# Kernel tuning notes

Measured on AMD Instinct MI355X. Metric: run time of the kernel, lower is better.

## Reference

```python
import jax, jax.numpy as jnp
import numpy as np

NUM_HEADS = 16
EPS = 1e-5
BLOCK = 16  # score_mod: q_idx // 16 == kv_idx % 16


def _ln(x, eps=EPS):
    # LayerNorm, elementwise_affine=False
    m = jnp.mean(x, axis=-1, keepdims=True)
    v = jnp.mean((x - m) ** 2, axis=-1, keepdims=True)
    return (x - m) * jax.lax.rsqrt(v + eps)


def setup_inputs() -> dict:
    key = jax.random.key(0)
    ks = jax.random.split(key, 5)
    N, D = 2048, 2048
    w = 0.02
    return {
        "x": jax.random.normal(ks[0], (N, D), jnp.float32),
        "Wq": jax.random.normal(ks[1], (D, D), jnp.float32) * w,
        "Wk": jax.random.normal(ks[2], (D, D), jnp.float32) * w,
        "Wv": jax.random.normal(ks[3], (D, D), jnp.float32) * w,
        "Wo": jax.random.normal(ks[4], (D, D), jnp.float32) * w,
    }


def reference(x, Wq, Wk, Wv, Wo):
    N, D = x.shape
    H = NUM_HEADS
    DH = D // H
    x_in = x
    xn = _ln(x)
    # per-head q/k layernorm, cast to attention dtype (bfloat16)
    q = _ln((xn @ Wq).reshape(N, H, DH)).astype(jnp.bfloat16)
    k = _ln((xn @ Wk).reshape(N, H, DH)).astype(jnp.bfloat16)
    v = (xn @ Wv).reshape(N, H, DH)  # stays fp32 (original applies no cast to vs)
    scale = 1.0 / np.sqrt(DH)
    # dense scores then sparsity mask, as flex_attention with score_mod does
    scores = jnp.einsum("nhd,mhd->hnm", q, k, preferred_element_type=jnp.float32) * scale
    qi = jnp.arange(N)
    mask = (qi[:, None] // BLOCK) == (qi[None, :] % BLOCK)  # [N, N]
    s = jnp.where(mask[None, :, :], scores, -jnp.inf)
    # safe softmax: rows with no allowed keys (q_idx >= 256) produce zeros
    mx = jnp.max(s, axis=-1, keepdims=True)
    e = jnp.exp(s - jnp.where(jnp.isfinite(mx), mx, 0.0))
    denom = jnp.sum(e, axis=-1, keepdims=True)
    attn = e / jnp.maximum(denom, 1e-30)
    o = jnp.einsum("hnm,mhd->nhd", attn, v)  # [N, H, DH]
    out = o.reshape(N, D) @ Wo
    return out + x_in
```

## Files before the change

### kernel.cpp

```cpp
#include <hip/hip_runtime.h>

typedef unsigned short u16;
typedef __attribute__((ext_vector_type(8))) short short8;
typedef __attribute__((ext_vector_type(4))) float f32x4;

#define D 2048
#define EPS 1e-5f

__device__ __forceinline__ u16 f2bf(float f) {
  unsigned u = __float_as_uint(f);
  u += 0x7fffu + ((u >> 16) & 1u);
  return (u16)(u >> 16);
}

__device__ __forceinline__ void async16(const void* g, void* l) {
  __builtin_amdgcn_global_load_lds(
      (const __attribute__((address_space(1))) void*)g,
      (__attribute__((address_space(3))) void*)l, 16, 0, 0);
}

__global__ __launch_bounds__(256) void prep(const float* __restrict__ x,
                                            const float* __restrict__ Wq,
                                            const float* __restrict__ Wk,
                                            const float* __restrict__ Wv,
                                            const float* __restrict__ Wo,
                                            u16* __restrict__ xn,
                                            float* __restrict__ out,
                                            u16* __restrict__ WqT, u16* __restrict__ WkT,
                                            u16* __restrict__ WvT, u16* __restrict__ WoT) {
  int bid = blockIdx.x;
  int t = threadIdx.x;
  if (bid < 2048) {
    const float* xr = x + (size_t)bid * D;
    float4 v[2];
    float s = 0.f, sq = 0.f;
#pragma unroll
    for (int i = 0; i < 2; i++) {
      v[i] = *(const float4*)(xr + i * 1024 + t * 4);
      s += v[i].x + v[i].y + v[i].z + v[i].w;
      sq += v[i].x * v[i].x + v[i].y * v[i].y + v[i].z * v[i].z + v[i].w * v[i].w;
    }
#pragma unroll
    for (int m = 32; m >= 1; m >>= 1) { s += __shfl_xor(s, m); sq += __shfl_xor(sq, m); }
    __shared__ float ps[4], pq[4];
    int w = t >> 6, lane = t & 63;
    if (lane == 0) { ps[w] = s; pq[w] = sq; }
    __syncthreads();
    s = ps[0] + ps[1] + ps[2] + ps[3];
    sq = pq[0] + pq[1] + pq[2] + pq[3];
    float mean = s * (1.f / D);
    float var = sq * (1.f / D) - mean * mean;
    float rs = rsqrtf(var + EPS);
    float* outr = out + (size_t)bid * D;
    u16* xnr = xn + (size_t)bid * D;
#pragma unroll
    for (int i = 0; i < 2; i++) {
      *(float4*)(outr + i * 1024 + t * 4) = v[i];
      ushort4 o;
      o.x = f2bf((v[i].x - mean) * rs);
      o.y = f2bf((v[i].y - mean) * rs);
      o.z = f2bf((v[i].z - mean) * rs);
      o.w = f2bf((v[i].w - mean) * rs);
      *(ushort4*)(xnr + i * 1024 + t * 4) = o;
    }
  } else {
    int tb = bid - 2048;
    int wsel = tb >> 10;
    int tt = tb & 1023;
    const float* src; u16* dst;
    switch (wsel) {
      case 0: src = Wq; dst = WqT; break;
      case 1: src = Wk; dst = WkT; break;
      case 2: src = Wv; dst = WvT; break;
      default: src = Wo; dst = WoT; break;
    }
    int i0 = (tt >> 5) * 64, j0 = (tt & 31) * 64;
    __shared__ u16 tile[64 * 66];
#pragma unroll
    for (int r = 0; r < 4; r++) {
      int idx = r * 256 + t;
      int row = idx >> 4, c4 = idx & 15;
      float4 v = *(const float4*)(src + (size_t)(i0 + row) * D + j0 + c4 * 4);
      tile[row * 66 + c4 * 4 + 0] = f2bf(v.x);
      tile[row * 66 + c4 * 4 + 1] = f2bf(v.y);
      tile[row * 66 + c4 * 4 + 2] = f2bf(v.z);
      tile[row * 66 + c4 * 4 + 3] = f2bf(v.w);
    }
    __syncthreads();
#pragma unroll
    for (int r = 0; r < 4; r++) {
      int idx = r * 256 + t;
      int row = idx >> 4, c4 = idx & 15;
      ushort4 o;
      o.x = tile[(c4 * 4 + 0) * 66 + row];
      o.y = tile[(c4 * 4 + 1) * 66 + row];
      o.z = tile[(c4 * 4 + 2) * 66 + row];
      o.w = tile[(c4 * 4 + 3) * 66 + row];
      *(ushort4*)(dst + (size_t)(j0 + row) * D + i0 + c4 * 4) = o;
    }
  }
}

__device__ __forceinline__ void gemm_tile(const u16* __restrict__ A,
                                          const u16* __restrict__ Bt,
                                          bool permB, int m0, int n0,
                                          int kbeg, int kend,
                                          u16* As, u16* Bs, f32x4 acc[4][4]) {
  int tid = threadIdx.x, wid = tid >> 6, lane = tid & 63;
  int q4 = lane >> 4, m16 = lane & 15;
  int wm = wid >> 1, wn = wid & 1;
  for (int kb = kbeg; kb < kend; kb += 64) {
#pragma unroll
    for (int p = 0; p < 4; p++) {
      int idx = p * 256 + tid;
      int r = idx >> 3, sl = idx & 7;
      int gc = sl ^ (r & 7);
      async16(A + (size_t)(m0 + r) * D + kb + gc * 8, As + (size_t)(p * 256 + wid * 64) * 8);
      int rb = n0 + r;
      int gr = permB ? ((rb & 127) * 16 + (rb >> 7)) : rb;
      async16(Bt + (size_t)gr * D + kb + gc * 8, Bs + (size_t)(p * 256 + wid * 64) * 8);
    }
    __syncthreads();
#pragma unroll
    for (int ks = 0; ks < 2; ks++) {
      short8 af[4], bf[4];
      int c = ks * 4 + q4;
#pragma unroll
      for (int i = 0; i < 4; i++) {
        int ra = wm * 64 + i * 16 + m16;
        af[i] = *(const short8*)(As + ra * 64 + (c ^ (ra & 7)) * 8);
        int rb = wn * 64 + i * 16 + m16;
        bf[i] = *(const short8*)(Bs + rb * 64 + (c ^ (rb & 7)) * 8);
      }
#pragma unroll
      for (int i = 0; i < 4; i++)
#pragma unroll
        for (int j = 0; j < 4; j++)
          acc[i][j] = __builtin_amdgcn_mfma_f32_16x16x32_bf16(af[i], bf[j], acc[i][j], 0, 0, 0);
    }
    __syncthreads();
  }
}

__global__ __launch_bounds__(256, 3) void gemm_mega(const u16* __restrict__ xn,
                                                    const u16* __restrict__ WkT,
                                                    const u16* __restrict__ WvT,
                                                    u16* __restrict__ K3,
                                                    u16* __restrict__ V3) {
  __shared__ u16 smem[2 * 128 * 64];
  u16* As = smem;
  u16* Bs = smem + 8192;
  int bid0 = blockIdx.x;
  int bid = (bid0 & 7) * 64 + (bid0 >> 3);
  int sel = bid >> 8;
  int z = bid & 255;
  int m0 = (z >> 4) * 128, n0 = (z & 15) * 128;
  const u16* A = sel ? WvT : xn;
  const u16* Bt = sel ? xn : WkT;
  f32x4 acc[4][4];
#pragma unroll
  for (int i = 0; i < 4; i++)
#pragma unroll
    for (int j = 0; j < 4; j++)
#pragma unroll
      for (int r = 0; r < 4; r++) acc[i][j][r] = 0.f;
  gemm_tile(A, Bt, sel == 1, m0, n0, 0, D, As, Bs, acc);

  int tid = threadIdx.x, wid = tid >> 6, lane = tid & 63;
  int q4 = lane >> 4, m16 = lane & 15;
  int wm = wid >> 1, wn = wid & 1;
  if (sel == 1) {
    int h = m0 >> 7, b = n0 >> 7;
#pragma unroll
    for (int i = 0; i < 4; i++)
#pragma unroll
      for (int j = 0; j < 4; j++)
#pragma unroll
        for (int r = 0; r < 4; r++) {
          int dhl = wm * 64 + i * 16 + q4 * 4 + r;
          int key = wn * 64 + j * 16 + m16;
          V3[((size_t)(h * 16 + b) * 128 + dhl) * 128 + key] = f2bf(acc[i][j][r]);
        }
  } else {
    float* redS = (float*)smem;
    float* redQ = redS + 256;
    __syncthreads();
#pragma unroll
    for (int i = 0; i < 4; i++) {
      float ps[4], pq[4];
#pragma unroll
      for (int r = 0; r < 4; r++) {
        float s = 0.f, q = 0.f;
#pragma unroll
        for (int j = 0; j < 4; j++) { float a = acc[i][j][r]; s += a; q += a * a; }
#pragma unroll
        for (int msk = 1; msk < 16; msk <<= 1) {
          s += __shfl_xor(s, msk);
          q += __shfl_xor(q, msk);
        }
        ps[r] = s; pq[r] = q;
      }
      if (m16 == 0) {
#pragma unroll
        for (int r = 0; r < 4; r++) {
          int row = wm * 64 + i * 16 + q4 * 4 + r;
          redS[row * 2 + wn] = ps[r];
          redQ[row * 2 + wn] = pq[r];
        }
      }
    }
    __syncthreads();
    int h = n0 >> 7;
#pragma unroll
    for (int i = 0; i < 4; i++)
#pragma unroll
      for (int r = 0; r < 4; r++) {
        int row = wm * 64 + i * 16 + q4 * 4 + r;
        float S = redS[row * 2] + redS[row * 2 + 1];
        float Qs = redQ[row * 2] + redQ[row * 2 + 1];
        float mean = S * (1.f / 128.f);
        float var = Qs * (1.f / 128.f) - mean * mean;
        float rstd = rsqrtf(var + EPS);
        int tok = m0 + row;
#pragma unroll
        for (int j = 0; j < 4; j++) {
          int dhl = wn * 64 + j * 16 + m16;
          u16 val = f2bf((acc[i][j][r] - mean) * rstd);
          K3[(((size_t)(h * 16 + (tok & 15))) * 128 + (tok >> 4)) * 128 + dhl] = val;
        }
      }
  }
}

__global__ __launch_bounds__(256) void attn(const u16* __restrict__ xn,
                                            const u16* __restrict__ WqT,
                                            const u16* __restrict__ K3,
                                            const u16* __restrict__ V3,
                                            u16* __restrict__ Ob) {
  int bh = blockIdx.x;
  int h = bh & 15, b = bh >> 4;
  int tid = threadIdx.x, w = tid >> 6, lane = tid & 63;
  int q4 = lane >> 4, m16 = lane & 15;
  __shared__ u16 Qs[16][136];
  __shared__ u16 P[16][136];
  __shared__ float redA[16][4];
  __shared__ float redB[16][4];
  __shared__ float redmx[4][16];
  __shared__ float redsm[4][16];
  __shared__ float invd[16];
  const float scale = 0.08838834764831845f;
  const u16* Ktile = K3 + (size_t)(h * 16 + b) * 128 * 128;
  const u16* Vtile = V3 + (size_t)(h * 16 + b) * 128 * 128;

  f32x4 qa[2];
#pragma unroll
  for (int nt = 0; nt < 2; nt++)
#pragma unroll
    for (int r = 0; r < 4; r++) qa[nt][r] = 0.f;
  const u16* xr = xn + (size_t)(b * 16 + m16) * D + q4 * 8;
  const u16* wr = WqT + (size_t)(h * 128 + w * 32 + m16) * D + q4 * 8;
#pragma unroll 4
  for (int kk = 0; kk < D; kk += 32) {
    short8 a = *(const short8*)(xr + kk);
    short8 b0 = *(const short8*)(wr + kk);
    short8 b1 = *(const short8*)(wr + 16 * D + kk);
    qa[0] = __builtin_amdgcn_mfma_f32_16x16x32_bf16(a, b0, qa[0], 0, 0, 0);
    qa[1] = __builtin_amdgcn_mfma_f32_16x16x32_bf16(a, b1, qa[1], 0, 0, 0);
  }
#pragma unroll
  for (int r = 0; r < 4; r++) {
    float s = qa[0][r] + qa[1][r];
    float q2 = qa[0][r] * qa[0][r] + qa[1][r] * qa[1][r];
#pragma unroll
    for (int msk = 1; msk < 16; msk <<= 1) { s += __shfl_xor(s, msk); q2 += __shfl_xor(q2, msk); }
    if (m16 == 0) { redA[q4 * 4 + r][w] = s; redB[q4 * 4 + r][w] = q2; }
  }
  __syncthreads();
#pragma unroll
  for (int r = 0; r < 4; r++) {
    int row = q4 * 4 + r;
    float S = redA[row][0] + redA[row][1] + redA[row][2] + redA[row][3];
    float Q2 = redB[row][0] + redB[row][1] + redB[row][2] + redB[row][3];
    float mean = S * (1.f / 128.f);
    float var = Q2 * (1.f / 128.f) - mean * mean;
    float rstd = rsqrtf(var + EPS);
#pragma unroll
    for (int nt = 0; nt < 2; nt++)
      Qs[row][w * 32 + nt * 16 + m16] = f2bf((qa[nt][r] - mean) * rstd);
  }
  __syncthreads();

  short8 af[4];
#pragma unroll
  for (int dc = 0; dc < 4; dc++)
    af[dc] = *(const short8*)(&Qs[m16][dc * 32 + q4 * 8]);
  f32x4 s[2];
#pragma unroll
  for (int kt = 0; kt < 2; kt++)
#pragma unroll
    for (int r = 0; r < 4; r++) s[kt][r] = 0.f;
#pragma unroll
  for (int kt = 0; kt < 2; kt++) {
    int key = w * 32 + kt * 16 + m16;
#pragma unroll
    for (int dc = 0; dc < 4; dc++) {
      short8 bf = *(const short8*)(Ktile + (size_t)key * 128 + dc * 32 + q4 * 8);
      s[kt] = __builtin_amdgcn_mfma_f32_16x16x32_bf16(af[dc], bf, s[kt], 0, 0, 0);
    }
  }
  float mx[4];
#pragma unroll
  for (int r = 0; r < 4; r++) {
    mx[r] = fmaxf(s[0][r], s[1][r]);
#pragma unroll
    for (int msk = 1; msk < 16; msk <<= 1) mx[r] = fmaxf(mx[r], __shfl_xor(mx[r], msk));
    if (m16 == 0) redmx[w][q4 * 4 + r] = mx[r];
  }
  __syncthreads();
#pragma unroll
  for (int r = 0; r < 4; r++) {
    int row = q4 * 4 + r;
    float M = fmaxf(fmaxf(redmx[0][row], redmx[1][row]), fmaxf(redmx[2][row], redmx[3][row]));
    float acc = 0.f;
#pragma unroll
    for (int kt = 0; kt < 2; kt++) {
      float e = __expf((s[kt][r] - M) * scale);
      s[kt][r] = e;
      acc += e;
    }
#pragma unroll
    for (int msk = 1; msk < 16; msk <<= 1) acc += __shfl_xor(acc, msk);
    if (m16 == 0) redsm[w][row] = acc;
  }
#pragma unroll
  for (int kt = 0; kt < 2; kt++)
#pragma unroll
    for (int r = 0; r < 4; r++)
      P[q4 * 4 + r][w * 32 + kt * 16 + m16] = f2bf(s[kt][r]);
  __syncthreads();
  if (tid < 16) invd[tid] = 1.0f / (redsm[0][tid] + redsm[1][tid] + redsm[2][tid] + redsm[3][tid]);
  __syncthreads();

  short8 pf[4];
#pragma unroll
  for (int kc = 0; kc < 4; kc++)
    pf[kc] = *(const short8*)(&P[m16][kc * 32 + q4 * 8]);
  f32x4 o[2];
#pragma unroll
  for (int dt = 0; dt < 2; dt++)
#pragma unroll
    for (int r = 0; r < 4; r++) o[dt][r] = 0.f;
#pragma unroll
  for (int dt = 0; dt < 2; dt++) {
    int dhl = w * 32 + dt * 16 + m16;
#pragma unroll
    for (int kc = 0; kc < 4; kc++) {
      short8 vf = *(const short8*)(Vtile + (size_t)dhl * 128 + kc * 32 + q4 * 8);
      o[dt] = __builtin_amdgcn_mfma_f32_16x16x32_bf16(pf[kc], vf, o[dt], 0, 0, 0);
    }
  }
#pragma unroll
  for (int dt = 0; dt < 2; dt++)
#pragma unroll
    for (int r = 0; r < 4; r++) {
      int row = q4 * 4 + r;
      float val = o[dt][r] * invd[row];
      Ob[(size_t)(b * 16 + row) * D + h * 128 + w * 32 + dt * 16 + m16] = f2bf(val);
    }
}

__global__ __launch_bounds__(256, 3) void gemm_wo(const u16* __restrict__ Ob,
                                                  const u16* __restrict__ WoT,
                                                  float* __restrict__ Wpart) {
  __shared__ u16 smem[2 * 128 * 64];
  u16* As = smem;
  u16* Bs = smem + 8192;
  int m0 = blockIdx.x * 128, n0 = blockIdx.y * 128;
  int z = blockIdx.z;
  int k0 = z * 256;
  f32x4 acc[4][4];
#pragma unroll
  for (int i = 0; i < 4; i++)
#pragma unroll
    for (int j = 0; j < 4; j++)
#pragma unroll
      for (int r = 0; r < 4; r++) acc[i][j][r] = 0.f;
  gemm_tile(Ob, WoT, false, m0, n0, k0, k0 + 256, As, Bs, acc);
  float* C = Wpart + (size_t)z * 256 * D;
  int tid = threadIdx.x, wid = tid >> 6, lane = tid & 63;
  int q4 = lane >> 4, m16 = lane & 15;
  int wm = wid >> 1, wn = wid & 1;
#pragma unroll
  for (int i = 0; i < 4; i++)
#pragma unroll
    for (int j = 0; j < 4; j++)
#pragma unroll
      for (int r = 0; r < 4; r++) {
        int row = m0 + wm * 64 + i * 16 + q4 * 4 + r;
        int col = n0 + wn * 64 + j * 16 + m16;
        C[(size_t)row * D + col] = acc[i][j][r];
      }
}

__global__ __launch_bounds__(256) void reduce_wo(const float* __restrict__ Wpart,
                                                 float* __restrict__ out) {
  int i = (blockIdx.x * 256 + threadIdx.x) * 4;
  float4 s = *(const float4*)(out + i);
#pragma unroll
  for (int z = 0; z < 8; z++) {
    float4 p = *(const float4*)(Wpart + (size_t)z * 256 * D + i);
    s.x += p.x; s.y += p.y; s.z += p.z; s.w += p.w;
  }
  *(float4*)(out + i) = s;
}

extern "C" void kernel_launch(void* const* d_in, const int* in_sizes, int n_in,
                              void* d_out, int out_size, void* d_ws, size_t ws_size,
                              hipStream_t stream) {
  const float* x  = (const float*)d_in[0];
  const float* Wq = (const float*)d_in[1];
  const float* Wk = (const float*)d_in[2];
  const float* Wv = (const float*)d_in[3];
  const float* Wo = (const float*)d_in[4];
  float* out = (float*)d_out;
  char* w = (char*)d_ws;
  const size_t MB = 1u << 20;
  u16*   xn    = (u16*)(w);
  u16*   WqT   = (u16*)(w + 8 * MB);
  u16*   WkT   = (u16*)(w + 16 * MB);
  u16*   WvT   = (u16*)(w + 24 * MB);
  u16*   WoT   = (u16*)(w + 32 * MB);
  u16*   K3    = (u16*)(w + 40 * MB);
  u16*   V3    = (u16*)(w + 48 * MB);
  u16*   Obf   = (u16*)(w + 56 * MB);
  float* Wpart = (float*)(w + 58 * MB);

  prep<<<dim3(6144), dim3(256), 0, stream>>>(x, Wq, Wk, Wv, Wo, xn, out, WqT, WkT, WvT, WoT);
  gemm_mega<<<dim3(512), dim3(256), 0, stream>>>(xn, WkT, WvT, K3, V3);
  attn<<<dim3(256), dim3(256), 0, stream>>>(xn, WqT, K3, V3, Obf);
  gemm_wo<<<dim3(2, 16, 8), dim3(256), 0, stream>>>(Obf, WoT, Wpart);
  reduce_wo<<<dim3(512), dim3(256), 0, stream>>>(Wpart, out);
}
```

Before: 207.3 us.

## Move Q projection into split-K tiles of the mega GEMM kernel

The Q projection for the 256 active query rows is taken out of the attention kernel. There, each block streamed its own 128x2048 slice of WqT straight from global memory with no LDS reuse. It now runs as 256 extra blocks in gemm_mega, using the shared LDS-tiled gemm_tile with an 8-way K split, and writes fp32 partials that the attention kernel sums before applying the per-head LayerNorm. This trades redundant global reads and a long serial MFMA loop for an extra 16MB of fp32 partial writes and reads. The partial buffer reuses the Wpart workspace region.

```diff
diff --git a/kernel.cpp b/kernel.cpp
--- a/kernel.cpp
+++ b/kernel.cpp
@@ -145,12 +145,44 @@
 __global__ __launch_bounds__(256, 3) void gemm_mega(const u16* __restrict__ xn,
                                                     const u16* __restrict__ WkT,
                                                     const u16* __restrict__ WvT,
+                                                    const u16* __restrict__ WqT,
                                                     u16* __restrict__ K3,
-                                                    u16* __restrict__ V3) {
+                                                    u16* __restrict__ V3,
+                                                    float* __restrict__ Qp) {
   __shared__ u16 smem[2 * 128 * 64];
   u16* As = smem;
   u16* Bs = smem + 8192;
   int bid0 = blockIdx.x;
+  int tid = threadIdx.x, wid = tid >> 6, lane = tid & 63;
+  int q4 = lane >> 4, m16 = lane & 15;
+  int wm = wid >> 1, wn = wid & 1;
+
+  if (bid0 >= 512) {
+    int qb = bid0 - 512;
+    int ks = qb & 7, t = qb >> 3;
+    int m0 = (t >> 4) * 128, n0 = (t & 15) * 128;
+    f32x4 acc[4][4];
+#pragma unroll
+    for (int i = 0; i < 4; i++)
+#pragma unroll
+      for (int j = 0; j < 4; j++)
+#pragma unroll
+        for (int r = 0; r < 4; r++) acc[i][j][r] = 0.f;
+    gemm_tile(xn, WqT, false, m0, n0, ks * 256, ks * 256 + 256, As, Bs, acc);
+    float* C = Qp + (size_t)ks * 256 * D;
+#pragma unroll
+    for (int i = 0; i < 4; i++)
+#pragma unroll
+      for (int j = 0; j < 4; j++)
+#pragma unroll
+        for (int r = 0; r < 4; r++) {
+          int row = m0 + wm * 64 + i * 16 + q4 * 4 + r;
+          int col = n0 + wn * 64 + j * 16 + m16;
+          C[(size_t)row * D + col] = acc[i][j][r];
+        }
+    return;
+  }
+
   int bid = (bid0 & 7) * 64 + (bid0 >> 3);
   int sel = bid >> 8;
   int z = bid & 255;
@@ -166,9 +198,6 @@
       for (int r = 0; r < 4; r++) acc[i][j][r] = 0.f;
   gemm_tile(A, Bt, sel == 1, m0, n0, 0, D, As, Bs, acc);
 
-  int tid = threadIdx.x, wid = tid >> 6, lane = tid & 63;
-  int q4 = lane >> 4, m16 = lane & 15;
-  int wm = wid >> 1, wn = wid & 1;
   if (sel == 1) {
     int h = m0 >> 7, b = n0 >> 7;
 #pragma unroll
@@ -232,8 +261,7 @@
   }
 }
 
-__global__ __launch_bounds__(256) void attn(const u16* __restrict__ xn,
-                                            const u16* __restrict__ WqT,
+__global__ __launch_bounds__(256) void attn(const float* __restrict__ Qp,
                                             const u16* __restrict__ K3,
                                             const u16* __restrict__ V3,
                                             u16* __restrict__ Ob) {
@@ -243,8 +271,6 @@
   int q4 = lane >> 4, m16 = lane & 15;
   __shared__ u16 Qs[16][136];
   __shared__ u16 P[16][136];
-  __shared__ float redA[16][4];
-  __shared__ float redB[16][4];
   __shared__ float redmx[4][16];
   __shared__ float redsm[4][16];
   __shared__ float invd[16];
@@ -252,41 +278,30 @@
   const u16* Ktile = K3 + (size_t)(h * 16 + b) * 128 * 128;
   const u16* Vtile = V3 + (size_t)(h * 16 + b) * 128 * 128;
 
-  f32x4 qa[2];
-#pragma unroll
-  for (int nt = 0; nt < 2; nt++)
-#pragma unroll
-    for (int r = 0; r < 4; r++) qa[nt][r] = 0.f;
-  const u16* xr = xn + (size_t)(b * 16 + m16) * D + q4 * 8;
-  const u16* wr = WqT + (size_t)(h * 128 + w * 32 + m16) * D + q4 * 8;
-#pragma unroll 4
-  for (int kk = 0; kk < D; kk += 32) {
-    short8 a = *(const short8*)(xr + kk);
-    short8 b0 = *(const short8*)(wr + kk);
-    short8 b1 = *(const short8*)(wr + 16 * D + kk);
-    qa[0] = __builtin_amdgcn_mfma_f32_16x16x32_bf16(a, b0, qa[0], 0, 0, 0);
-    qa[1] = __builtin_amdgcn_mfma_f32_16x16x32_bf16(a, b1, qa[1], 0, 0, 0);
-  }
-#pragma unroll
-  for (int r = 0; r < 4; r++) {
-    float s = qa[0][r] + qa[1][r];
-    float q2 = qa[0][r] * qa[0][r] + qa[1][r] * qa[1][r];
-#pragma unroll
-    for (int msk = 1; msk < 16; msk <<= 1) { s += __shfl_xor(s, msk); q2 += __shfl_xor(q2, msk); }
-    if (m16 == 0) { redA[q4 * 4 + r][w] = s; redB[q4 * 4 + r][w] = q2; }
-  }
-  __syncthreads();
-#pragma unroll
-  for (int r = 0; r < 4; r++) {
-    int row = q4 * 4 + r;
-    float S = redA[row][0] + redA[row][1] + redA[row][2] + redA[row][3];
-    float Q2 = redB[row][0] + redB[row][1] + redB[row][2] + redB[row][3];
-    float mean = S * (1.f / 128.f);
-    float var = Q2 * (1.f / 128.f) - mean * mean;
+  {
+    int row = tid >> 4;
+    int c8 = (tid & 15) * 8;
+    const float* qpb = Qp + (size_t)(b * 16 + row) * D + h * 128 + c8;
+    float q8[8];
+#pragma unroll
+    for (int ii = 0; ii < 8; ii++) q8[ii] = 0.f;
+#pragma unroll
+    for (int ks = 0; ks < 8; ks++) {
+      float4 a = *(const float4*)(qpb + (size_t)ks * 256 * D);
+      float4 bb = *(const float4*)(qpb + (size_t)ks * 256 * D + 4);
+      q8[0] += a.x; q8[1] += a.y; q8[2] += a.z; q8[3] += a.w;
+      q8[4] += bb.x; q8[5] += bb.y; q8[6] += bb.z; q8[7] += bb.w;
+    }
+    float s = 0.f, sq = 0.f;
+#pragma unroll
+    for (int ii = 0; ii < 8; ii++) { s += q8[ii]; sq += q8[ii] * q8[ii]; }
+#pragma unroll
+    for (int msk = 1; msk < 16; msk <<= 1) { s += __shfl_xor(s, msk); sq += __shfl_xor(sq, msk); }
+    float mean = s * (1.f / 128.f);
+    float var = sq * (1.f / 128.f) - mean * mean;
     float rstd = rsqrtf(var + EPS);
 #pragma unroll
-    for (int nt = 0; nt < 2; nt++)
-      Qs[row][w * 32 + nt * 16 + m16] = f2bf((qa[nt][r] - mean) * rstd);
+    for (int ii = 0; ii < 8; ii++) Qs[row][c8 + ii] = f2bf((q8[ii] - mean) * rstd);
   }
   __syncthreads();
 
@@ -433,11 +448,12 @@
   u16*   K3    = (u16*)(w + 40 * MB);
   u16*   V3    = (u16*)(w + 48 * MB);
   u16*   Obf   = (u16*)(w + 56 * MB);
+  float* Qp    = (float*)(w + 58 * MB);
   float* Wpart = (float*)(w + 58 * MB);
 
   prep<<<dim3(6144), dim3(256), 0, stream>>>(x, Wq, Wk, Wv, Wo, xn, out, WqT, WkT, WvT, WoT);
-  gemm_mega<<<dim3(512), dim3(256), 0, stream>>>(xn, WkT, WvT, K3, V3);
-  attn<<<dim3(256), dim3(256), 0, stream>>>(xn, WqT, K3, V3, Obf);
+  gemm_mega<<<dim3(768), dim3(256), 0, stream>>>(xn, WkT, WvT, WqT, K3, V3, Qp);
+  attn<<<dim3(256), dim3(256), 0, stream>>>(Qp, K3, V3, Obf);
   gemm_wo<<<dim3(2, 16, 8), dim3(256), 0, stream>>>(Obf, WoT, Wpart);
   reduce_wo<<<dim3(512), dim3(256), 0, stream>>>(Wpart, out);
 }
```

Result: faster. 191.5 us (-7.6%).
